# Kernel tuning notes

Measured on AMD Instinct MI355X. Metric: run time of the kernel, lower is better.

## Reference

```python
import jax, jax.numpy as jnp
import numpy as np

B, L, C = 32, 2880, 862
PRED, SEG = 720, 48
NUM_MAP, K, STRIDE = 4, 16, 8
N_IN, N_OUT = L // SEG, PRED // SEG          # 60, 15
CONV_DIM = (L - K) // STRIDE + 1             # 359


def setup_inputs() -> dict:
    key = jax.random.key(0)
    ks = jax.random.split(key, 4)
    s = 0.05
    return {
        "x": jax.random.normal(ks[0], (B, L, C), jnp.float32),
        "conv_w": jax.random.normal(ks[1], (C, 1, K), jnp.float32) * s,   # per-channel depthwise kernels
        "conv_b": jnp.zeros((C,), jnp.float32),
        "gate_w": jax.random.normal(ks[2], (NUM_MAP, CONV_DIM), jnp.float32) * s,
        "gate_b": jnp.zeros((NUM_MAP,), jnp.float32),
        "map_w": jax.random.normal(ks[3], (NUM_MAP, N_OUT, N_IN), jnp.float32) * s,
        "map_b": jnp.zeros((NUM_MAP, N_OUT), jnp.float32),
    }


def reference(x, conv_w, conv_b, gate_w, gate_b, map_w, map_b):
    # [B, L, C] -> [B, C, L]
    xt = jnp.transpose(x, (0, 2, 1))
    # RevIN-style normalize (means detached, as in torch .detach())
    means = jax.lax.stop_gradient(jnp.mean(xt, axis=2, keepdims=True))
    xc = xt - means
    stdev = jnp.sqrt(jnp.var(xc, axis=2, keepdims=True) + 1e-10)  # biased var, eps=1e-10
    xn = xc / stdev                                               # [B, C, L]
    # c independent per-channel Conv1d == grouped conv with feature_group_count=C
    conv = jax.lax.conv_general_dilated(
        xn, conv_w, window_strides=(STRIDE,), padding='VALID',
        dimension_numbers=('NCH', 'OIH', 'NCH'), feature_group_count=C)
    conv = conv + conv_b[None, :, None]                           # [B, C, CONV_DIM]
    # softmax gating over num_map experts
    gates = jax.nn.softmax(jnp.einsum('bcd,md->bcm', conv, gate_w) + gate_b, axis=-1)  # [B, C, M]
    # segment view: [B, C, N_IN, SEG] -> [B, C, SEG, N_IN]
    xseg = jnp.transpose(xn.reshape(B, C, N_IN, SEG), (0, 1, 3, 2))
    # all num_map linear experts in one batched contraction: [B, C, M, N_OUT, SEG]
    y = jnp.einsum('bcsi,moi->bcmos', xseg, map_w) + map_b[None, None, :, :, None]
    y = y.reshape(B, C, NUM_MAP, PRED)                            # flatten (N_OUT, SEG) -> PRED
    out = jnp.einsum('bcms,bcm->bcs', y, gates)                   # gated combine
    # denormalize and back to [B, PRED, C]
    out = out * stdev + means
    return jnp.transpose(out, (0, 2, 1))
```

## Files before the change

### kernel.cpp

```cpp
#include <hip/hip_runtime.h>
#include <cstdint>
#include <cstddef>

#define NB 32
#define NL 2880
#define NC_TOT 862
#define NPRED 720
#define NSEG 48
#define NMAP 4
#define NK 16
#define NIN 60
#define NOUT 15
#define NCONV 359

__global__ __launch_bounds__(256) void k1_stats_gates(
    const float* __restrict__ x,
    const float* __restrict__ conv_w,
    const float* __restrict__ conv_b,
    const float* __restrict__ gate_w,
    const float* __restrict__ gate_b,
    float* __restrict__ ws2)
{
  __shared__ __align__(16) float gw[NCONV * 4];
  __shared__ float red[6][8][32];
  __shared__ float g1s[4];

  const int tid = threadIdx.x;

  for (int idx = tid; idx < NMAP * NCONV; idx += 256) {
    int m = idx / NCONV;
    int d = idx - m * NCONV;
    gw[d * 4 + m] = gate_w[idx];
  }
  __syncthreads();

  if (tid < 64) {
    float p0 = 0.f, p1 = 0.f, p2 = 0.f, p3 = 0.f;
    for (int d = tid; d < NCONV; d += 64) {
      p0 += gw[d * 4 + 0];
      p1 += gw[d * 4 + 1];
      p2 += gw[d * 4 + 2];
      p3 += gw[d * 4 + 3];
    }
    #pragma unroll
    for (int off = 32; off > 0; off >>= 1) {
      p0 += __shfl_down(p0, off, 64);
      p1 += __shfl_down(p1, off, 64);
      p2 += __shfl_down(p2, off, 64);
      p3 += __shfl_down(p3, off, 64);
    }
    if (tid == 0) { g1s[0] = p0; g1s[1] = p1; g1s[2] = p2; g1s[3] = p3; }
  }

  const int cl = tid & 31;
  const int q  = tid >> 5;
  const int c  = blockIdx.x * 32 + cl;
  const int b  = blockIdx.y;
  const bool active = (c < NC_TOT);

  float sum = 0.f, sumsq = 0.f;
  float gacc0 = 0.f, gacc1 = 0.f, gacc2 = 0.f, gacc3 = 0.f;
  float Sw = 0.f;

  if (active) {
    const float* xp = x + (size_t)b * NL * NC_TOT + c;
    float w[NK];
    #pragma unroll
    for (int k = 0; k < NK; ++k) { w[k] = conv_w[c * NK + k]; Sw += w[k]; }

    float A[8], Bv[8];
    const int d0 = q * 45;
    const int d1 = (q == 7) ? NCONV : (d0 + 45);
    const int dlast = q * 45 + 44;

    #pragma unroll
    for (int j = 0; j < 8; ++j) {
      float v = xp[(size_t)(d0 * 8 + j) * NC_TOT];
      A[j] = v; sum += v; sumsq = fmaf(v, v, sumsq);
    }
    for (int d = d0; d < d1; ++d) {
      #pragma unroll
      for (int j = 0; j < 8; ++j)
        Bv[j] = xp[(size_t)(d * 8 + 8 + j) * NC_TOT];
      if (d != dlast) {
        #pragma unroll
        for (int j = 0; j < 8; ++j) { sum += Bv[j]; sumsq = fmaf(Bv[j], Bv[j], sumsq); }
      }
      float cr = 0.f;
      #pragma unroll
      for (int j = 0; j < 8; ++j) cr = fmaf(A[j], w[j], cr);
      #pragma unroll
      for (int j = 0; j < 8; ++j) cr = fmaf(Bv[j], w[j + 8], cr);
      const float4 g4 = *(const float4*)&gw[d * 4];
      gacc0 = fmaf(cr, g4.x, gacc0);
      gacc1 = fmaf(cr, g4.y, gacc1);
      gacc2 = fmaf(cr, g4.z, gacc2);
      gacc3 = fmaf(cr, g4.w, gacc3);
      #pragma unroll
      for (int j = 0; j < 8; ++j) A[j] = Bv[j];
    }
  }

  red[0][q][cl] = sum;
  red[1][q][cl] = sumsq;
  red[2][q][cl] = gacc0;
  red[3][q][cl] = gacc1;
  red[4][q][cl] = gacc2;
  red[5][q][cl] = gacc3;
  __syncthreads();

  if (tid < 32 && active) {
    float t[6];
    #pragma unroll
    for (int cc = 0; cc < 6; ++cc) {
      float s = 0.f;
      #pragma unroll
      for (int qq = 0; qq < 8; ++qq) s += red[cc][qq][tid];
      t[cc] = s;
    }
    const float mean = t[0] * (1.0f / NL);
    const float var  = t[1] * (1.0f / NL) - mean * mean;
    const float sd   = sqrtf(var + 1e-10f);
    const float rstd = 1.0f / sd;
    const float cb   = conv_b[c];
    const float k0   = cb - rstd * mean * Sw;
    float lg[4];
    lg[0] = rstd * t[2] + k0 * g1s[0] + gate_b[0];
    lg[1] = rstd * t[3] + k0 * g1s[1] + gate_b[1];
    lg[2] = rstd * t[4] + k0 * g1s[2] + gate_b[2];
    lg[3] = rstd * t[5] + k0 * g1s[3] + gate_b[3];
    const float mx = fmaxf(fmaxf(lg[0], lg[1]), fmaxf(lg[2], lg[3]));
    const float e0 = expf(lg[0] - mx);
    const float e1 = expf(lg[1] - mx);
    const float e2 = expf(lg[2] - mx);
    const float e3 = expf(lg[3] - mx);
    const float inv = 1.0f / (e0 + e1 + e2 + e3);

    const size_t cs = (size_t)NB * NC_TOT;
    float* o2 = ws2 + (size_t)b * NC_TOT + c;
    o2[0 * cs] = mean;
    o2[1 * cs] = sd;
    o2[2 * cs] = e0 * inv;
    o2[3 * cs] = e1 * inv;
    o2[4 * cs] = e2 * inv;
    o2[5 * cs] = e3 * inv;
  }
}

__global__ __launch_bounds__(384) void k2_out(
    const float* __restrict__ x,
    const float* __restrict__ map_w,
    const float* __restrict__ map_b,
    const float* __restrict__ ws2,
    float* __restrict__ out)
{
  __shared__ __align__(16) float weff[16 * 900];
  __shared__ float sgl[6][16];
  __shared__ float beff[16 * 16];

  const int tid = threadIdx.x;
  const int b  = blockIdx.y;
  const int c0 = blockIdx.x * 16;
  const size_t cs = (size_t)NB * NC_TOT;

  if (tid < 6 * 16) {
    int comp = tid >> 4;
    int cl   = tid & 15;
    int cc   = c0 + cl;
    if (cc > NC_TOT - 1) cc = NC_TOT - 1;
    sgl[comp][cl] = ws2[comp * cs + (size_t)b * NC_TOT + cc];
  }
  __syncthreads();

  for (int idx = tid; idx < 16 * 900; idx += 384) {
    int cl = idx / 900;
    int oi = idx - cl * 900;
    weff[idx] = sgl[2][cl] * map_w[oi]
              + sgl[3][cl] * map_w[900  + oi]
              + sgl[4][cl] * map_w[1800 + oi]
              + sgl[5][cl] * map_w[2700 + oi];
  }
  if (tid < 16 * NOUT) {
    int cl = tid / NOUT;
    int o  = tid - cl * NOUT;
    beff[cl * 16 + o] = sgl[2][cl] * map_b[o]
                      + sgl[3][cl] * map_b[15 + o]
                      + sgl[4][cl] * map_b[30 + o]
                      + sgl[5][cl] * map_b[45 + o];
  }
  __syncthreads();

  const int cl = tid & 15;
  const int sg = tid >> 4;
  const int c  = c0 + cl;
  const bool active = (c < NC_TOT);
  const float mean = sgl[0][cl];
  const float sd   = sgl[1][cl];

  float xa[NIN], xb[NIN];
  const float* xp = x + (size_t)b * NL * NC_TOT + c;
  if (active) {
    #pragma unroll
    for (int i = 0; i < NIN; ++i) {
      xa[i] = xp[(size_t)(i * 48 + sg) * NC_TOT] - mean;
      xb[i] = xp[(size_t)(i * 48 + sg + 24) * NC_TOT] - mean;
    }
  } else {
    #pragma unroll
    for (int i = 0; i < NIN; ++i) { xa[i] = 0.f; xb[i] = 0.f; }
  }

  float* op = out + (size_t)b * NPRED * NC_TOT + c;
  const float* wrow = &weff[cl * 900];
  for (int o = 0; o < NOUT; ++o) {
    float aa = 0.f, ab = 0.f;
    #pragma unroll
    for (int i4 = 0; i4 < 15; ++i4) {
      const float4 w4 = *(const float4*)&wrow[o * 60 + i4 * 4];
      aa = fmaf(xa[i4 * 4 + 0], w4.x, aa);
      aa = fmaf(xa[i4 * 4 + 1], w4.y, aa);
      aa = fmaf(xa[i4 * 4 + 2], w4.z, aa);
      aa = fmaf(xa[i4 * 4 + 3], w4.w, aa);
      ab = fmaf(xb[i4 * 4 + 0], w4.x, ab);
      ab = fmaf(xb[i4 * 4 + 1], w4.y, ab);
      ab = fmaf(xb[i4 * 4 + 2], w4.z, ab);
      ab = fmaf(xb[i4 * 4 + 3], w4.w, ab);
    }
    const float cst = fmaf(sd, beff[cl * 16 + o], mean);
    if (active) {
      op[(size_t)(o * 48 + sg) * NC_TOT]      = aa + cst;
      op[(size_t)(o * 48 + sg + 24) * NC_TOT] = ab + cst;
    }
  }
}

extern "C" void kernel_launch(void* const* d_in, const int* in_sizes, int n_in,
                              void* d_out, int out_size, void* d_ws, size_t ws_size,
                              hipStream_t stream)
{
  (void)in_sizes; (void)n_in; (void)out_size; (void)ws_size;
  const float* x      = (const float*)d_in[0];
  const float* conv_w = (const float*)d_in[1];
  const float* conv_b = (const float*)d_in[2];
  const float* gate_w = (const float*)d_in[3];
  const float* gate_b = (const float*)d_in[4];
  const float* map_w  = (const float*)d_in[5];
  const float* map_b  = (const float*)d_in[6];
  float* out = (float*)d_out;
  float* ws2 = (float*)d_ws;

  dim3 g1((NC_TOT + 31) / 32, NB), b1(256);
  hipLaunchKernelGGL(k1_stats_gates, g1, b1, 0, stream,
                     x, conv_w, conv_b, gate_w, gate_b, ws2);

  dim3 g2((NC_TOT + 15) / 16, NB), b2(384);
  hipLaunchKernelGGL(k2_out, g2, b2, 0, stream,
                     x, map_w, map_b, ws2, out);
}
```

Baseline: 656.8 us.

## Restructure output kernel to use shared raw map weights and pipelined loads

The output kernel stops building per-channel gated effective weights in shared memory. It keeps the four raw expert weight matrices in shared memory and applies the gate to x on the fly, with the mean correction folded into a precomputed row-sum constant. Each thread now covers three segment positions for 32 channels in 512-thread blocks, and x loads are double-buffered across input-segment chunks. This removes most of the shared-memory setup and allows more blocks per CU, at the cost of four times more FMAs per output and a larger register footprint from the 45 accumulators.

```diff
diff --git a/kernel.cpp b/kernel.cpp
--- a/kernel.cpp
+++ b/kernel.cpp
@@ -147,89 +147,113 @@
   }
 }
 
-__global__ __launch_bounds__(384) void k2_out(
+#define K2_LOADCH(BUF, I4)                                                   \
+  {                                                                          \
+    _Pragma("unroll") for (int j = 0; j < 4; ++j) {                          \
+      const size_t r = (size_t)(((I4) * 4 + j) * 48 + 3 * sg) * NC_TOT;      \
+      BUF[j * 3 + 0] = xp[r];                                                \
+      BUF[j * 3 + 1] = xp[r + NC_TOT];                                       \
+      BUF[j * 3 + 2] = xp[r + 2 * NC_TOT];                                   \
+    }                                                                        \
+  }
+
+#define K2_COMPUTE(XV, I4)                                                   \
+  {                                                                          \
+    _Pragma("unroll") for (int m = 0; m < 4; ++m) {                          \
+      const float gm = gv[m];                                                \
+      float xg[12];                                                          \
+      _Pragma("unroll") for (int t = 0; t < 12; ++t) xg[t] = XV[t] * gm;     \
+      _Pragma("unroll") for (int o = 0; o < 15; ++o) {                       \
+        const float4 w4 =                                                    \
+            *(const float4*)&mw[m * 900 + o * 60 + (I4) * 4];                \
+        _Pragma("unroll") for (int k = 0; k < 3; ++k) {                      \
+          float a = acc[o][k];                                               \
+          a = fmaf(xg[0 * 3 + k], w4.x, a);                                  \
+          a = fmaf(xg[1 * 3 + k], w4.y, a);                                  \
+          a = fmaf(xg[2 * 3 + k], w4.z, a);                                  \
+          a = fmaf(xg[3 * 3 + k], w4.w, a);                                  \
+          acc[o][k] = a;                                                     \
+        }                                                                    \
+      }                                                                      \
+    }                                                                        \
+  }
+
+__global__ __launch_bounds__(512, 4) void k2_out(
     const float* __restrict__ x,
     const float* __restrict__ map_w,
     const float* __restrict__ map_b,
     const float* __restrict__ ws2,
     float* __restrict__ out)
 {
-  __shared__ __align__(16) float weff[16 * 900];
-  __shared__ float sgl[6][16];
-  __shared__ float beff[16 * 16];
+  __shared__ __align__(16) float mw[NMAP * NOUT * NIN];
+  __shared__ float mwsum[NMAP][16];
+  __shared__ float mb[NMAP][16];
 
   const int tid = threadIdx.x;
-  const int b  = blockIdx.y;
-  const int c0 = blockIdx.x * 16;
-  const size_t cs = (size_t)NB * NC_TOT;
-
-  if (tid < 6 * 16) {
-    int comp = tid >> 4;
-    int cl   = tid & 15;
-    int cc   = c0 + cl;
-    if (cc > NC_TOT - 1) cc = NC_TOT - 1;
-    sgl[comp][cl] = ws2[comp * cs + (size_t)b * NC_TOT + cc];
-  }
-  __syncthreads();
-
-  for (int idx = tid; idx < 16 * 900; idx += 384) {
-    int cl = idx / 900;
-    int oi = idx - cl * 900;
-    weff[idx] = sgl[2][cl] * map_w[oi]
-              + sgl[3][cl] * map_w[900  + oi]
-              + sgl[4][cl] * map_w[1800 + oi]
-              + sgl[5][cl] * map_w[2700 + oi];
-  }
-  if (tid < 16 * NOUT) {
-    int cl = tid / NOUT;
-    int o  = tid - cl * NOUT;
-    beff[cl * 16 + o] = sgl[2][cl] * map_b[o]
-                      + sgl[3][cl] * map_b[15 + o]
-                      + sgl[4][cl] * map_b[30 + o]
-                      + sgl[5][cl] * map_b[45 + o];
-  }
-  __syncthreads();
-
-  const int cl = tid & 15;
-  const int sg = tid >> 4;
+  const int b   = blockIdx.y;
+  const int c0  = blockIdx.x * 32;
+
+  const int cl = tid & 31;
+  const int sg = tid >> 5;
   const int c  = c0 + cl;
   const bool active = (c < NC_TOT);
-  const float mean = sgl[0][cl];
-  const float sd   = sgl[1][cl];
-
-  float xa[NIN], xb[NIN];
-  const float* xp = x + (size_t)b * NL * NC_TOT + c;
-  if (active) {
-    #pragma unroll
-    for (int i = 0; i < NIN; ++i) {
-      xa[i] = xp[(size_t)(i * 48 + sg) * NC_TOT] - mean;
-      xb[i] = xp[(size_t)(i * 48 + sg + 24) * NC_TOT] - mean;
-    }
-  } else {
-    #pragma unroll
-    for (int i = 0; i < NIN; ++i) { xa[i] = 0.f; xb[i] = 0.f; }
-  }
-
-  float* op = out + (size_t)b * NPRED * NC_TOT + c;
-  const float* wrow = &weff[cl * 900];
+  const int cc = active ? c : (NC_TOT - 1);
+
+  const size_t cs = (size_t)NB * NC_TOT;
+  const float* wsb = ws2 + (size_t)b * NC_TOT + cc;
+  const float mean = wsb[0 * cs];
+  const float sd   = wsb[1 * cs];
+  const float gv[4] = { wsb[2 * cs], wsb[3 * cs], wsb[4 * cs], wsb[5 * cs] };
+
+  const float* xp = x + (size_t)b * NL * NC_TOT + cc;
+
+  float xv0[12], xv1[12];
+  K2_LOADCH(xv0, 0);
+
+  for (int idx = tid; idx < 900; idx += 512) {
+    ((float4*)mw)[idx] = ((const float4*)map_w)[idx];
+  }
+  __syncthreads();
+
+  if (tid < 64) {
+    const int m = tid >> 4, o = tid & 15;
+    if (o < NOUT) {
+      float s = 0.f;
+      #pragma unroll
+      for (int i = 0; i < NIN; ++i) s += mw[m * 900 + o * 60 + i];
+      mwsum[m][o] = s;
+      mb[m][o] = map_b[m * NOUT + o];
+    }
+  }
+  __syncthreads();
+
+  float acc[NOUT][3];
+  #pragma unroll
+  for (int o = 0; o < NOUT; ++o)
+    #pragma unroll
+    for (int k = 0; k < 3; ++k) acc[o][k] = 0.f;
+
+  #pragma unroll 1
+  for (int i4 = 0; i4 < 14; i4 += 2) {
+    K2_LOADCH(xv1, i4 + 1);
+    K2_COMPUTE(xv0, i4);
+    K2_LOADCH(xv0, i4 + 2);
+    K2_COMPUTE(xv1, i4 + 1);
+  }
+  K2_COMPUTE(xv0, 14);
+
+  float* op = out + (size_t)b * NPRED * NC_TOT + cc;
+  #pragma unroll
   for (int o = 0; o < NOUT; ++o) {
-    float aa = 0.f, ab = 0.f;
-    #pragma unroll
-    for (int i4 = 0; i4 < 15; ++i4) {
-      const float4 w4 = *(const float4*)&wrow[o * 60 + i4 * 4];
-      aa = fmaf(xa[i4 * 4 + 0], w4.x, aa);
-      aa = fmaf(xa[i4 * 4 + 1], w4.y, aa);
-      aa = fmaf(xa[i4 * 4 + 2], w4.z, aa);
-      aa = fmaf(xa[i4 * 4 + 3], w4.w, aa);
-      ab = fmaf(xb[i4 * 4 + 0], w4.x, ab);
-      ab = fmaf(xb[i4 * 4 + 1], w4.y, ab);
-      ab = fmaf(xb[i4 * 4 + 2], w4.z, ab);
-      ab = fmaf(xb[i4 * 4 + 3], w4.w, ab);
-    }
-    const float cst = fmaf(sd, beff[cl * 16 + o], mean);
+    float gwo = gv[0] * mwsum[0][o] + gv[1] * mwsum[1][o]
+              + gv[2] * mwsum[2][o] + gv[3] * mwsum[3][o];
+    float gbo = gv[0] * mb[0][o] + gv[1] * mb[1][o]
+              + gv[2] * mb[2][o] + gv[3] * mb[3][o];
+    const float cst = fmaf(-mean, gwo, fmaf(sd, gbo, mean));
     if (active) {
-      op[(size_t)(o * 48 + sg) * NC_TOT]      = aa + cst;
-      op[(size_t)(o * 48 + sg + 24) * NC_TOT] = ab + cst;
+      #pragma unroll
+      for (int k = 0; k < 3; ++k)
+        op[(size_t)(o * 48 + 3 * sg + k) * NC_TOT] = acc[o][k] + cst;
     }
   }
 }
@@ -253,7 +277,7 @@
   hipLaunchKernelGGL(k1_stats_gates, g1, b1, 0, stream,
                      x, conv_w, conv_b, gate_w, gate_b, ws2);
 
-  dim3 g2((NC_TOT + 15) / 16, NB), b2(384);
+  dim3 g2((NC_TOT + 31) / 32, NB), b2(512);
   hipLaunchKernelGGL(k2_out, g2, b2, 0, stream,
                      x, map_w, map_b, ws2, out);
 }
```

Result: slower. 1.206 ms (+83.6%).
